# Optimization experiments

Hardware: AMD Instinct MI355X
Metric: run time of the kernel (lower is better)

Reference implementation:

```python
import jax, jax.numpy as jnp
import numpy as np

NUM_TOKENS_SCORE = 64
NUM_HEADS = 16
NUM_KV_HEADS = 4
HEAD_SIZE = 128
SCALE = 0.08838834764831845  # 1/sqrt(128)


def setup_inputs() -> dict:
    key = jax.random.key(0)
    k1, k2, k3 = jax.random.split(key, 3)
    B, S = 2, 2048
    total = B * S
    return {
        "query": jax.random.normal(k1, (total, NUM_HEADS * HEAD_SIZE), dtype=jnp.float32),
        "key": jax.random.normal(k2, (total, NUM_KV_HEADS * HEAD_SIZE), dtype=jnp.float32),
        "value": jax.random.normal(k3, (total, NUM_KV_HEADS * HEAD_SIZE), dtype=jnp.float32),
        "batch_size": B,
        "seq_len": S,
    }


def reference(query, key, value, batch_size, seq_len):
    """Prompt-phase SparsePagedAttention: varlen causal GQA attention (equal
    prompt lengths -> dense [B,S] layout) plus the fused softmax score-sum over
    the last NUM_TOKENS_SCORE query rows used for KV-cache pruning."""
    B, S = batch_size, seq_len
    H, Hk, D = NUM_HEADS, NUM_KV_HEADS, HEAD_SIZE
    rep = H // Hk  # queries per kv head (head_mapping via repeat_interleave)

    q = query.reshape(B, S, H, D)
    k = jnp.repeat(key.reshape(B, S, Hk, D), rep, axis=2)    # [B,S,H,D]
    v = jnp.repeat(value.reshape(B, S, Hk, D), rep, axis=2)  # [B,S,H,D]

    scores = jnp.einsum('bqhd,bkhd->bhqk', q, k) * SCALE      # [B,H,S,S]
    causal = jnp.tril(jnp.ones((S, S), dtype=bool))
    scores = jnp.where(causal[None, None], scores, jnp.finfo(scores.dtype).min)
    probs = jax.nn.softmax(scores, axis=-1)                   # [B,H,S,S]

    out = jnp.einsum('bhqk,bkhd->bqhd', probs, v).reshape(B * S, H * D)
    # triton_fused_softmax_sum: sum softmax probs over last NUM_TOKENS_SCORE queries
    score_sum = probs[:, :, S - NUM_TOKENS_SCORE:, :].sum(axis=2)  # [B,H,S]
    return out, score_sum
```

## Files before the change

kernel.cpp:

```cpp
#include <hip/hip_runtime.h>


#define BB 2
#define SS 2048
#define NH 16
#define NKV 4
#define DD 128
#define TILE_SH 4096

typedef __attribute__((ext_vector_type(8))) short bf16x8;
typedef __attribute__((ext_vector_type(4))) float f32x4;

constexpr float SCL = 0.08838834764831845f * 1.4426950408889634f;

__device__ __forceinline__ short f2bf(float f) {
  union { float f; unsigned u; } v; v.f = f;
  unsigned r = v.u + 0x7FFFu + ((v.u >> 16) & 1u);
  return (short)(r >> 16);
}

__device__ __forceinline__ unsigned pack2bf(float a, float b) {
  union { float f; unsigned u; } x, y; x.f = a; y.f = b;
  return __builtin_amdgcn_perm(y.u, x.u, 0x07060302);
}

__device__ __forceinline__ void gl_lds16(const void* g, void* l) {
  __builtin_amdgcn_global_load_lds(
      (const __attribute__((address_space(1))) unsigned*)g,
      (__attribute__((address_space(3))) unsigned*)l, 16, 0, 0);
}

__global__ void prep(const float* __restrict__ K, const float* __restrict__ V,
                     short* __restrict__ Kb, short* __restrict__ Vb) {
  const int p = blockIdx.x;
  const int b = p >> 8, hk = (p >> 6) & 3, kt = p & 63;
  const int tid = threadIdx.x;
  const int k0 = kt * 32;
  short* kb = Kb + ((size_t)((b * 4 + hk) * 64 + kt)) * TILE_SH;
  short* vb = Vb + ((size_t)((b * 4 + hk) * 64 + kt)) * TILE_SH;
  {
    const int k = tid & 31, chb = tid >> 5;
    const float* src = K + ((size_t)(b * SS + k0 + k) * NKV + hk) * DD;
#pragma unroll
    for (int i = 0; i < 2; ++i) {
      const int ch = chb + i * 8;
      const float* s = src + ch * 8;
      float4 f0 = *(const float4*)s;
      float4 f1 = *(const float4*)(s + 4);
      bf16x8 t;
      t[0] = f2bf(f0.x); t[1] = f2bf(f0.y); t[2] = f2bf(f0.z); t[3] = f2bf(f0.w);
      t[4] = f2bf(f1.x); t[5] = f2bf(f1.y); t[6] = f2bf(f1.z); t[7] = f2bf(f1.w);
      *(bf16x8*)(kb + (ch * 32 + k) * 8) = t;
    }
  }
  {
    const int d = tid & 127, kcb = tid >> 7;
#pragma unroll
    for (int i = 0; i < 2; ++i) {
      const int kc = kcb + i * 2;
      const float* s = V + ((size_t)(b * SS + k0 + kc * 8) * NKV + hk) * DD + d;
      bf16x8 t;
#pragma unroll
      for (int e = 0; e < 8; ++e) t[e] = f2bf(s[(size_t)e * (NKV * DD)]);
      *(bf16x8*)(vb + (kc * 128 + d) * 8) = t;
    }
  }
}

__global__ __launch_bounds__(256, 4) void fa2(
    const float* __restrict__ Q, const short* __restrict__ Kb,
    const short* __restrict__ Vb, float* __restrict__ Out,
    float* __restrict__ wsl) {
  __shared__ bf16x8 kv[2][1024];
  __shared__ short ldsP[4][640];

  const int tid = threadIdx.x;
  const int w = tid >> 6, lane = tid & 63;
  const int c = lane & 15, qd = lane >> 4;

  const int i = blockIdx.x;
  const int g = i >> 8, cc = i & 255;
  const int bh = cc >> 3, jp = cc & 7;
  const int qt = (g == 0) ? jp : (g == 1) ? 31 - jp : (g == 2) ? 8 + jp : 23 - jp;
  const int b = bh >> 4, h = bh & 15, hk = h >> 2;

  const char* KT = (const char*)(Kb + ((size_t)(b * 4 + hk)) * 64 * TILE_SH);
  const char* VT = (const char*)(Vb + ((size_t)(b * 4 + hk)) * 64 * TILE_SH);

  auto stage = [&](int kt, int bi) {
    const char* sk = KT + (size_t)kt * 8192 + w * 2048 + lane * 16;
    const char* sv = VT + (size_t)kt * 8192 + w * 2048 + lane * 16;
    char* dk = (char*)kv[bi] + w * 2048;
    char* dv = dk + 8192;
#pragma unroll
    for (int t = 0; t < 2; ++t) {
      gl_lds16(sk + t * 1024, dk + t * 1024);
      gl_lds16(sv + t * 1024, dv + t * 1024);
    }
  };

  stage(0, 0);

  const int nk = 2 * qt + 2;

  const float* qrow = Q + ((size_t)(b * SS + qt * 64 + w * 16 + c) * NH + h) * DD;
  bf16x8 qf[4];
#pragma unroll
  for (int ks = 0; ks < 4; ++ks) {
    const float* p = qrow + ks * 32 + qd * 8;
    float4 f0 = *(const float4*)p;
    float4 f1 = *(const float4*)(p + 4);
    bf16x8 t;
    t[0] = f2bf(f0.x * SCL); t[1] = f2bf(f0.y * SCL);
    t[2] = f2bf(f0.z * SCL); t[3] = f2bf(f0.w * SCL);
    t[4] = f2bf(f1.x * SCL); t[5] = f2bf(f1.y * SCL);
    t[6] = f2bf(f1.z * SCL); t[7] = f2bf(f1.w * SCL);
    qf[ks] = t;
  }

  f32x4 o[8];
#pragma unroll
  for (int dt = 0; dt < 8; ++dt) { o[dt][0] = 0.f; o[dt][1] = 0.f; o[dt][2] = 0.f; o[dt][3] = 0.f; }
  float l_part = 0.f;

  for (int kt = 0; kt < nk; ++kt) {
    __syncthreads();
    const int cb = kt & 1;
    if (kt + 1 < nk) stage(kt + 1, cb ^ 1);

    const bf16x8* bK = kv[cb];
    const bf16x8* bV = kv[cb] + 512;

    f32x4 st0 = {0.f, 0.f, 0.f, 0.f}, st1 = {0.f, 0.f, 0.f, 0.f};
#pragma unroll
    for (int ks = 0; ks < 4; ++ks) {
      const int chz = (ks * 4 + qd) * 32;
      bf16x8 a0 = bK[chz + c];
      bf16x8 a1 = bK[chz + 16 + c];
      st0 = __builtin_amdgcn_mfma_f32_16x16x32_bf16(a0, qf[ks], st0, 0, 0, 0);
      st1 = __builtin_amdgcn_mfma_f32_16x16x32_bf16(a1, qf[ks], st1, 0, 0, 0);
    }

    float pr[8];
#pragma unroll
    for (int r = 0; r < 4; ++r) { pr[r] = exp2f(st0[r]); pr[4 + r] = exp2f(st1[r]); }
    const int koff = kt * 32 - qt * 64;
    if (koff >= 0) {
      const int qrl = w * 16 + c;
#pragma unroll
      for (int mt = 0; mt < 2; ++mt)
#pragma unroll
        for (int r = 0; r < 4; ++r)
          if (koff + mt * 16 + qd * 4 + r > qrl) pr[mt * 4 + r] = 0.f;
    }
#pragma unroll
    for (int x = 0; x < 8; ++x) l_part += pr[x];

    short* pp = ldsP[w] + c * 40;
#pragma unroll
    for (int mt = 0; mt < 2; ++mt) {
      union { short4 s4; unsigned u[2]; } pk;
      pk.u[0] = pack2bf(pr[mt * 4 + 0], pr[mt * 4 + 1]);
      pk.u[1] = pack2bf(pr[mt * 4 + 2], pr[mt * 4 + 3]);
      *(short4*)(pp + mt * 16 + qd * 4) = pk.s4;
    }
    __asm__ volatile("s_waitcnt lgkmcnt(0)" ::: "memory");
    bf16x8 pf = *(const bf16x8*)(pp + qd * 8);

#pragma unroll
    for (int dt = 0; dt < 8; ++dt)
      o[dt] = __builtin_amdgcn_mfma_f32_16x16x32_bf16(bV[qd * 128 + dt * 16 + c],
                                                      pf, o[dt], 0, 0, 0);
  }

  float l = l_part;
  l += __shfl_xor(l, 16);
  l += __shfl_xor(l, 32);
  const float linv = 1.f / l;

  float* orow = Out + ((size_t)(b * SS + qt * 64 + w * 16 + c) * NH + h) * DD;
#pragma unroll
  for (int dt = 0; dt < 8; ++dt) {
    float4 ov;
    ov.x = o[dt][0] * linv; ov.y = o[dt][1] * linv;
    ov.z = o[dt][2] * linv; ov.w = o[dt][3] * linv;
    *(float4*)(orow + dt * 16 + qd * 4) = ov;
  }
  if (qt == 31 && qd == 0)
    wsl[bh * 64 + w * 16 + c] = l;
}

__global__ __launch_bounds__(256, 2) void score(
    const float* __restrict__ Q, const short* __restrict__ Kb,
    const float* __restrict__ wsl, float* __restrict__ out2) {
  __shared__ float ldsS[4][64];
  const int tid = threadIdx.x;
  const int w = tid >> 6, lane = tid & 63;
  const int c = lane & 15, qd = lane >> 4;
  const int bh = blockIdx.x & 31, kt = blockIdx.x >> 5;
  const int b = bh >> 4, h = bh & 15, hk = h >> 2;
  const int q0 = SS - 64;

  const float* qrow = Q + ((size_t)(b * SS + q0 + w * 16 + c) * NH + h) * DD;
  bf16x8 qf[4];
#pragma unroll
  for (int ks = 0; ks < 4; ++ks) {
    const float* p = qrow + ks * 32 + qd * 8;
    float4 f0 = *(const float4*)p;
    float4 f1 = *(const float4*)(p + 4);
    bf16x8 t;
    t[0] = f2bf(f0.x * SCL); t[1] = f2bf(f0.y * SCL);
    t[2] = f2bf(f0.z * SCL); t[3] = f2bf(f0.w * SCL);
    t[4] = f2bf(f1.x * SCL); t[5] = f2bf(f1.y * SCL);
    t[6] = f2bf(f1.z * SCL); t[7] = f2bf(f1.w * SCL);
    qf[ks] = t;
  }
  float linv[4];
  const int r0 = bh * 64 + w * 16 + qd * 4;
#pragma unroll
  for (int r = 0; r < 4; ++r) linv[r] = 1.f / wsl[r0 + r];

  const bf16x8* kb = (const bf16x8*)Kb + ((size_t)(b * 4 + hk) * 64 + kt * 2) * 512;
  f32x4 s[4];
#pragma unroll
  for (int nt = 0; nt < 4; ++nt) { s[nt][0] = 0.f; s[nt][1] = 0.f; s[nt][2] = 0.f; s[nt][3] = 0.f; }
#pragma unroll
  for (int ks = 0; ks < 4; ++ks) {
#pragma unroll
    for (int nt = 0; nt < 4; ++nt) {
      bf16x8 kf = kb[(nt >> 1) * 512 + (ks * 4 + qd) * 32 + (nt & 1) * 16 + c];
      s[nt] = __builtin_amdgcn_mfma_f32_16x16x32_bf16(qf[ks], kf, s[nt], 0, 0, 0);
    }
  }
  const bool diag = (kt == 31);
  float cs[4] = {0.f, 0.f, 0.f, 0.f};
#pragma unroll
  for (int nt = 0; nt < 4; ++nt) {
#pragma unroll
    for (int r = 0; r < 4; ++r) {
      float pv = exp2f(s[nt][r]) * linv[r];
      if (diag && nt * 16 + c > w * 16 + qd * 4 + r) pv = 0.f;
      cs[nt] += pv;
    }
    cs[nt] += __shfl_xor(cs[nt], 16);
    cs[nt] += __shfl_xor(cs[nt], 32);
  }
  if (lane < 16) {
#pragma unroll
    for (int nt = 0; nt < 4; ++nt) ldsS[w][nt * 16 + c] = cs[nt];
  }
  __syncthreads();
  if (tid < 64)
    out2[(size_t)bh * SS + kt * 64 + tid] =
        ldsS[0][tid] + ldsS[1][tid] + ldsS[2][tid] + ldsS[3][tid];
}

extern "C" void kernel_launch(void* const* d_in, const int* in_sizes, int n_in,
                              void* d_out, int out_size, void* d_ws, size_t ws_size,
                              hipStream_t stream) {
  const float* Q = (const float*)d_in[0];
  const float* K = (const float*)d_in[1];
  const float* V = (const float*)d_in[2];
  float* out = (float*)d_out;
  float* out2 = out + (size_t)BB * SS * NH * DD;

  short* Kb = (short*)d_ws;
  const size_t tsz = (size_t)2 * 4 * 64 * TILE_SH;
  short* Vb = Kb + tsz;
  float* wsl = (float*)(Vb + tsz);

  hipLaunchKernelGGL(prep, dim3(512), dim3(256), 0, stream, K, V, Kb, Vb);
  hipLaunchKernelGGL(fa2, dim3(1024), dim3(256), 0, stream, Q, Kb, Vb, out, wsl);
  hipLaunchKernelGGL(score, dim3(1024), dim3(256), 0, stream, Q, Kb, wsl, out2);
}
```

Before: 162.4 us.

## Process two query sub-tiles per wave in fa2 with 128-thread blocks

The attention kernel now runs 2 waves per block instead of 4, and each wave handles 32 query rows as two 16-row sub-tiles. Each K/V fragment loaded from LDS now feeds two MFMAs, which halves LDS reads per unit of work, and each wave stages twice as much data. The block schedule changes from an interleaved balanced order to a simple heaviest-first order. Launch bounds on prep and score are also adjusted. The cost is higher register pressure from doubled accumulators and fewer waves per block to hide latency.

Result: slower. 177.0 us (+9.0%).

```diff
diff --git a/kernel.cpp b/kernel.cpp
--- a/kernel.cpp
+++ b/kernel.cpp
@@ -30,8 +30,9 @@
       (__attribute__((address_space(3))) unsigned*)l, 16, 0, 0);
 }
 
-__global__ void prep(const float* __restrict__ K, const float* __restrict__ V,
-                     short* __restrict__ Kb, short* __restrict__ Vb) {
+__global__ __launch_bounds__(256, 4) void prep(
+    const float* __restrict__ K, const float* __restrict__ V,
+    short* __restrict__ Kb, short* __restrict__ Vb) {
   const int p = blockIdx.x;
   const int b = p >> 8, hk = (p >> 6) & 3, kt = p & 63;
   const int tid = threadIdx.x;
@@ -67,7 +68,7 @@
   }
 }
 
-__global__ __launch_bounds__(256, 4) void fa2(
+__global__ __launch_bounds__(128, 2) void fa2(
     const float* __restrict__ Q, const short* __restrict__ Kb,
     const short* __restrict__ Vb, float* __restrict__ Out,
     float* __restrict__ wsl) {
@@ -79,21 +80,20 @@
   const int c = lane & 15, qd = lane >> 4;
 
   const int i = blockIdx.x;
-  const int g = i >> 8, cc = i & 255;
-  const int bh = cc >> 3, jp = cc & 7;
-  const int qt = (g == 0) ? jp : (g == 1) ? 31 - jp : (g == 2) ? 8 + jp : 23 - jp;
+  const int qt = 31 - (i >> 5);
+  const int bh = i & 31;
   const int b = bh >> 4, h = bh & 15, hk = h >> 2;
 
   const char* KT = (const char*)(Kb + ((size_t)(b * 4 + hk)) * 64 * TILE_SH);
   const char* VT = (const char*)(Vb + ((size_t)(b * 4 + hk)) * 64 * TILE_SH);
 
   auto stage = [&](int kt, int bi) {
-    const char* sk = KT + (size_t)kt * 8192 + w * 2048 + lane * 16;
-    const char* sv = VT + (size_t)kt * 8192 + w * 2048 + lane * 16;
-    char* dk = (char*)kv[bi] + w * 2048;
-    char* dv = dk + 8192;
-#pragma unroll
-    for (int t = 0; t < 2; ++t) {
+    const char* sk = KT + (size_t)kt * 8192 + w * 4096 + lane * 16;
+    const char* sv = VT + (size_t)kt * 8192 + w * 4096 + lane * 16;
+    char* dk = (char*)kv[bi] + w * 4096;
+    char* dv = (char*)kv[bi] + 8192 + w * 4096;
+#pragma unroll
+    for (int t = 0; t < 4; ++t) {
       gl_lds16(sk + t * 1024, dk + t * 1024);
       gl_lds16(sv + t * 1024, dv + t * 1024);
     }
@@ -103,7 +103,135 @@
 
   const int nk = 2 * qt + 2;
 
-  const float* qrow = Q + ((size_t)(b * SS + qt * 64 + w * 16 + c) * NH + h) * DD;
+  const float* qrA = Q + ((size_t)(b * SS + qt * 64 + w * 32 + c) * NH + h) * DD;
+  const float* qrB = qrA + (size_t)16 * NH * DD;
+  bf16x8 qfA[4], qfB[4];
+#pragma unroll
+  for (int ks = 0; ks < 4; ++ks) {
+    const float* pA = qrA + ks * 32 + qd * 8;
+    const float* pB = qrB + ks * 32 + qd * 8;
+    float4 a0 = *(const float4*)pA, a1 = *(const float4*)(pA + 4);
+    float4 b0 = *(const float4*)pB, b1 = *(const float4*)(pB + 4);
+    bf16x8 tA, tB;
+    tA[0] = f2bf(a0.x * SCL); tA[1] = f2bf(a0.y * SCL);
+    tA[2] = f2bf(a0.z * SCL); tA[3] = f2bf(a0.w * SCL);
+    tA[4] = f2bf(a1.x * SCL); tA[5] = f2bf(a1.y * SCL);
+    tA[6] = f2bf(a1.z * SCL); tA[7] = f2bf(a1.w * SCL);
+    tB[0] = f2bf(b0.x * SCL); tB[1] = f2bf(b0.y * SCL);
+    tB[2] = f2bf(b0.z * SCL); tB[3] = f2bf(b0.w * SCL);
+    tB[4] = f2bf(b1.x * SCL); tB[5] = f2bf(b1.y * SCL);
+    tB[6] = f2bf(b1.z * SCL); tB[7] = f2bf(b1.w * SCL);
+    qfA[ks] = tA; qfB[ks] = tB;
+  }
+
+  f32x4 oA[8], oB[8];
+#pragma unroll
+  for (int dt = 0; dt < 8; ++dt) {
+    oA[dt][0] = 0.f; oA[dt][1] = 0.f; oA[dt][2] = 0.f; oA[dt][3] = 0.f;
+    oB[dt][0] = 0.f; oB[dt][1] = 0.f; oB[dt][2] = 0.f; oB[dt][3] = 0.f;
+  }
+  float lA = 0.f, lB = 0.f;
+
+  for (int kt = 0; kt < nk; ++kt) {
+    __syncthreads();
+    const int cb = kt & 1;
+    if (kt + 1 < nk) stage(kt + 1, cb ^ 1);
+
+    const bf16x8* bK = kv[cb];
+    const bf16x8* bV = kv[cb] + 512;
+
+    f32x4 sA0 = {0.f, 0.f, 0.f, 0.f}, sA1 = {0.f, 0.f, 0.f, 0.f};
+    f32x4 sB0 = {0.f, 0.f, 0.f, 0.f}, sB1 = {0.f, 0.f, 0.f, 0.f};
+#pragma unroll
+    for (int ks = 0; ks < 4; ++ks) {
+      const int chz = (ks * 4 + qd) * 32;
+      bf16x8 a0 = bK[chz + c];
+      bf16x8 a1 = bK[chz + 16 + c];
+      sA0 = __builtin_amdgcn_mfma_f32_16x16x32_bf16(a0, qfA[ks], sA0, 0, 0, 0);
+      sB0 = __builtin_amdgcn_mfma_f32_16x16x32_bf16(a0, qfB[ks], sB0, 0, 0, 0);
+      sA1 = __builtin_amdgcn_mfma_f32_16x16x32_bf16(a1, qfA[ks], sA1, 0, 0, 0);
+      sB1 = __builtin_amdgcn_mfma_f32_16x16x32_bf16(a1, qfB[ks], sB1, 0, 0, 0);
+    }
+
+    float pA[8], pB[8];
+#pragma unroll
+    for (int r = 0; r < 4; ++r) {
+      pA[r] = exp2f(sA0[r]); pA[4 + r] = exp2f(sA1[r]);
+      pB[r] = exp2f(sB0[r]); pB[4 + r] = exp2f(sB1[r]);
+    }
+    const int koff = kt * 32 - qt * 64;
+    if (koff >= 0) {
+      const int qrlA = w * 32 + c, qrlB = qrlA + 16;
+#pragma unroll
+      for (int mt = 0; mt < 2; ++mt)
+#pragma unroll
+        for (int r = 0; r < 4; ++r) {
+          const int kc = koff + mt * 16 + qd * 4 + r;
+          if (kc > qrlA) pA[mt * 4 + r] = 0.f;
+          if (kc > qrlB) pB[mt * 4 + r] = 0.f;
+        }
+    }
+#pragma unroll
+    for (int x = 0; x < 8; ++x) { lA += pA[x]; lB += pB[x]; }
+
+    short* ppA = ldsP[w * 2 + 0] + c * 40;
+    short* ppB = ldsP[w * 2 + 1] + c * 40;
+#pragma unroll
+    for (int mt = 0; mt < 2; ++mt) {
+      union { short4 s4; unsigned u[2]; } ka, kb2;
+      ka.u[0] = pack2bf(pA[mt * 4 + 0], pA[mt * 4 + 1]);
+      ka.u[1] = pack2bf(pA[mt * 4 + 2], pA[mt * 4 + 3]);
+      kb2.u[0] = pack2bf(pB[mt * 4 + 0], pB[mt * 4 + 1]);
+      kb2.u[1] = pack2bf(pB[mt * 4 + 2], pB[mt * 4 + 3]);
+      *(short4*)(ppA + mt * 16 + qd * 4) = ka.s4;
+      *(short4*)(ppB + mt * 16 + qd * 4) = kb2.s4;
+    }
+    __asm__ volatile("s_waitcnt lgkmcnt(0)" ::: "memory");
+    bf16x8 pfA = *(const bf16x8*)(ppA + qd * 8);
+    bf16x8 pfB = *(const bf16x8*)(ppB + qd * 8);
+
+#pragma unroll
+    for (int dt = 0; dt < 8; ++dt) {
+      bf16x8 vf = bV[qd * 128 + dt * 16 + c];
+      oA[dt] = __builtin_amdgcn_mfma_f32_16x16x32_bf16(vf, pfA, oA[dt], 0, 0, 0);
+      oB[dt] = __builtin_amdgcn_mfma_f32_16x16x32_bf16(vf, pfB, oB[dt], 0, 0, 0);
+    }
+  }
+
+  lA += __shfl_xor(lA, 16); lA += __shfl_xor(lA, 32);
+  lB += __shfl_xor(lB, 16); lB += __shfl_xor(lB, 32);
+  const float liA = 1.f / lA, liB = 1.f / lB;
+
+  float* orA = Out + ((size_t)(b * SS + qt * 64 + w * 32 + c) * NH + h) * DD;
+  float* orB = orA + (size_t)16 * NH * DD;
+#pragma unroll
+  for (int dt = 0; dt < 8; ++dt) {
+    float4 va, vb2;
+    va.x = oA[dt][0] * liA; va.y = oA[dt][1] * liA;
+    va.z = oA[dt][2] * liA; va.w = oA[dt][3] * liA;
+    vb2.x = oB[dt][0] * liB; vb2.y = oB[dt][1] * liB;
+    vb2.z = oB[dt][2] * liB; vb2.w = oB[dt][3] * liB;
+    *(float4*)(orA + dt * 16 + qd * 4) = va;
+    *(float4*)(orB + dt * 16 + qd * 4) = vb2;
+  }
+  if (qt == 31 && qd == 0) {
+    wsl[bh * 64 + w * 32 + c] = lA;
+    wsl[bh * 64 + w * 32 + 16 + c] = lB;
+  }
+}
+
+__global__ __launch_bounds__(256, 4) void score(
+    const float* __restrict__ Q, const short* __restrict__ Kb,
+    const float* __restrict__ wsl, float* __restrict__ out2) {
+  __shared__ float ldsS[4][64];
+  const int tid = threadIdx.x;
+  const int w = tid >> 6, lane = tid & 63;
+  const int c = lane & 15, qd = lane >> 4;
+  const int bh = blockIdx.x & 31, kt = blockIdx.x >> 5;
+  const int b = bh >> 4, h = bh & 15, hk = h >> 2;
+  const int q0 = SS - 64;
+
+  const float* qrow = Q + ((size_t)(b * SS + q0 + w * 16 + c) * NH + h) * DD;
   bf16x8 qf[4];
 #pragma unroll
   for (int ks = 0; ks < 4; ++ks) {
@@ -117,104 +245,6 @@
     t[6] = f2bf(f1.z * SCL); t[7] = f2bf(f1.w * SCL);
     qf[ks] = t;
   }
-
-  f32x4 o[8];
-#pragma unroll
-  for (int dt = 0; dt < 8; ++dt) { o[dt][0] = 0.f; o[dt][1] = 0.f; o[dt][2] = 0.f; o[dt][3] = 0.f; }
-  float l_part = 0.f;
-
-  for (int kt = 0; kt < nk; ++kt) {
-    __syncthreads();
-    const int cb = kt & 1;
-    if (kt + 1 < nk) stage(kt + 1, cb ^ 1);
-
-    const bf16x8* bK = kv[cb];
-    const bf16x8* bV = kv[cb] + 512;
-
-    f32x4 st0 = {0.f, 0.f, 0.f, 0.f}, st1 = {0.f, 0.f, 0.f, 0.f};
-#pragma unroll
-    for (int ks = 0; ks < 4; ++ks) {
-      const int chz = (ks * 4 + qd) * 32;
-      bf16x8 a0 = bK[chz + c];
-      bf16x8 a1 = bK[chz + 16 + c];
-      st0 = __builtin_amdgcn_mfma_f32_16x16x32_bf16(a0, qf[ks], st0, 0, 0, 0);
-      st1 = __builtin_amdgcn_mfma_f32_16x16x32_bf16(a1, qf[ks], st1, 0, 0, 0);
-    }
-
-    float pr[8];
-#pragma unroll
-    for (int r = 0; r < 4; ++r) { pr[r] = exp2f(st0[r]); pr[4 + r] = exp2f(st1[r]); }
-    const int koff = kt * 32 - qt * 64;
-    if (koff >= 0) {
-      const int qrl = w * 16 + c;
-#pragma unroll
-      for (int mt = 0; mt < 2; ++mt)
-#pragma unroll
-        for (int r = 0; r < 4; ++r)
-          if (koff + mt * 16 + qd * 4 + r > qrl) pr[mt * 4 + r] = 0.f;
-    }
-#pragma unroll
-    for (int x = 0; x < 8; ++x) l_part += pr[x];
-
-    short* pp = ldsP[w] + c * 40;
-#pragma unroll
-    for (int mt = 0; mt < 2; ++mt) {
-      union { short4 s4; unsigned u[2]; } pk;
-      pk.u[0] = pack2bf(pr[mt * 4 + 0], pr[mt * 4 + 1]);
-      pk.u[1] = pack2bf(pr[mt * 4 + 2], pr[mt * 4 + 3]);
-      *(short4*)(pp + mt * 16 + qd * 4) = pk.s4;
-    }
-    __asm__ volatile("s_waitcnt lgkmcnt(0)" ::: "memory");
-    bf16x8 pf = *(const bf16x8*)(pp + qd * 8);
-
-#pragma unroll
-    for (int dt = 0; dt < 8; ++dt)
-      o[dt] = __builtin_amdgcn_mfma_f32_16x16x32_bf16(bV[qd * 128 + dt * 16 + c],
-                                                      pf, o[dt], 0, 0, 0);
-  }
-
-  float l = l_part;
-  l += __shfl_xor(l, 16);
-  l += __shfl_xor(l, 32);
-  const float linv = 1.f / l;
-
-  float* orow = Out + ((size_t)(b * SS + qt * 64 + w * 16 + c) * NH + h) * DD;
-#pragma unroll
-  for (int dt = 0; dt < 8; ++dt) {
-    float4 ov;
-    ov.x = o[dt][0] * linv; ov.y = o[dt][1] * linv;
-    ov.z = o[dt][2] * linv; ov.w = o[dt][3] * linv;
-    *(float4*)(orow + dt * 16 + qd * 4) = ov;
-  }
-  if (qt == 31 && qd == 0)
-    wsl[bh * 64 + w * 16 + c] = l;
-}
-
-__global__ __launch_bounds__(256, 2) void score(
-    const float* __restrict__ Q, const short* __restrict__ Kb,
-    const float* __restrict__ wsl, float* __restrict__ out2) {
-  __shared__ float ldsS[4][64];
-  const int tid = threadIdx.x;
-  const int w = tid >> 6, lane = tid & 63;
-  const int c = lane & 15, qd = lane >> 4;
-  const int bh = blockIdx.x & 31, kt = blockIdx.x >> 5;
-  const int b = bh >> 4, h = bh & 15, hk = h >> 2;
-  const int q0 = SS - 64;
-
-  const float* qrow = Q + ((size_t)(b * SS + q0 + w * 16 + c) * NH + h) * DD;
-  bf16x8 qf[4];
-#pragma unroll
-  for (int ks = 0; ks < 4; ++ks) {
-    const float* p = qrow + ks * 32 + qd * 8;
-    float4 f0 = *(const float4*)p;
-    float4 f1 = *(const float4*)(p + 4);
-    bf16x8 t;
-    t[0] = f2bf(f0.x * SCL); t[1] = f2bf(f0.y * SCL);
-    t[2] = f2bf(f0.z * SCL); t[3] = f2bf(f0.w * SCL);
-    t[4] = f2bf(f1.x * SCL); t[5] = f2bf(f1.y * SCL);
-    t[6] = f2bf(f1.z * SCL); t[7] = f2bf(f1.w * SCL);
-    qf[ks] = t;
-  }
   float linv[4];
   const int r0 = bh * 64 + w * 16 + qd * 4;
 #pragma unroll
@@ -270,6 +300,6 @@
   float* wsl = (float*)(Vb + tsz);
 
   hipLaunchKernelGGL(prep, dim3(512), dim3(256), 0, stream, K, V, Kb, Vb);
-  hipLaunchKernelGGL(fa2, dim3(1024), dim3(256), 0, stream, Q, Kb, Vb, out, wsl);
+  hipLaunchKernelGGL(fa2, dim3(1024), dim3(128), 0, stream, Q, Kb, Vb, out, wsl);
   hipLaunchKernelGGL(score, dim3(1024), dim3(256), 0, stream, Q, Kb, wsl, out2);
 }
```
